# Optimization experiments

Measured on AMD Instinct MI355X. Metric: run time of the kernel, lower is better.

The kernel has to match this reference:

```python
import jax, jax.numpy as jnp
import numpy as np

N = 50000
E = 800000
F = 128


def gcn_smooth(edge_index, x):
    """Symmetric-normalized GCN smoothing: D^-1/2 (A + I) D^-1/2 x.

    edge_index: [2, E] int (src, dst) of a sparse graph; self-loops added here.
    x: [N, F] float node features.
    """
    src, dst = edge_index[0], edge_index[1]
    n = x.shape[0]
    # degree of A + I
    deg = jax.ops.segment_sum(jnp.ones((src.shape[0],), x.dtype), dst, num_segments=n) + 1.0
    dinv = jax.lax.rsqrt(deg)  # [N]
    # per-edge normalization d^-1/2[src] * d^-1/2[dst]
    norm_e = dinv[src] * dinv[dst]  # [E]
    msg = x[src] * norm_e[:, None]  # [E, F] -- gather + scale
    agg = jax.ops.segment_sum(msg, dst, num_segments=n)  # scatter-add over dst
    # self-loop contribution: dinv[i]^2 * x[i]
    return agg + (dinv * dinv)[:, None] * x


def setup_inputs() -> dict:
    key = jax.random.key(0)
    ks = jax.random.split(key, 12)
    inp = {
        "X_HypGNet": jax.random.normal(ks[0], (N, F), jnp.float32),
        "X_CGNet": jax.random.normal(ks[1], (N, F), jnp.float32),
        "X_SGNet": jax.random.normal(ks[2], (N, F), jnp.float32),
        "edge_index_hyp": jax.random.randint(ks[3], (2, E), 0, N, dtype=jnp.int32),
        "edge_index_c": jax.random.randint(ks[4], (2, E), 0, N, dtype=jnp.int32),
        "edge_index_s": jax.random.randint(ks[5], (2, E), 0, N, dtype=jnp.int32),
        "W_hyp": jax.random.normal(ks[6], (F, F), jnp.float32) * 0.05,
        "b_hyp": jax.random.normal(ks[7], (F,), jnp.float32) * 0.05,
        "W_cg": jax.random.normal(ks[8], (F, F), jnp.float32) * 0.05,
        "b_cg": jax.random.normal(ks[9], (F,), jnp.float32) * 0.05,
        "W_sg": jax.random.normal(ks[10], (F, F), jnp.float32) * 0.05,
        "b_sg": jax.random.normal(ks[11], (F,), jnp.float32) * 0.05,
    }
    return inp


def reference(X_HypGNet, X_CGNet, X_SGNet, edge_index_hyp, edge_index_c, edge_index_s,
              W_hyp, b_hyp, W_cg, b_cg, W_sg, b_sg):
    X_hyp = X_HypGNet @ W_hyp + b_hyp
    X_cg = X_CGNet @ W_cg + b_cg
    X_sg = X_SGNet @ W_sg + b_sg
    X_hyp_s = gcn_smooth(edge_index_hyp, X_hyp)
    X_cg_s = gcn_smooth(edge_index_c, X_cg)
    X_sg_s = gcn_smooth(edge_index_s, X_sg)
    return (X_hyp_s, X_cg_s, X_sg_s)
```

## Files before the change

kernel.cpp:

```cpp
#include <hip/hip_runtime.h>

#define F_DIM 128
#define NG 3
#define AEPT 16
#define CAP 48
#define MAXBIN 256
#define SPILL_CAP 8192

typedef __attribute__((ext_vector_type(8))) short short8_t;
typedef __attribute__((ext_vector_type(4))) float f32x4;

__device__ __forceinline__ unsigned short f2bf(float f) {
    unsigned int x = __float_as_uint(f);
    unsigned int r = x + 0x7fffu + ((x >> 16) & 1u);
    return (unsigned short)(r >> 16);
}
__device__ __forceinline__ float bflo(unsigned int u) { return __uint_as_float(u << 16); }
__device__ __forceinline__ float bfhi(unsigned int u) { return __uint_as_float(u & 0xffff0000u); }

__device__ __forceinline__ short8_t cvt8(float4 x0, float4 x1) {
    union { short8_t s; uint4 u; } pk;
    pk.u.x = (unsigned)f2bf(x0.x) | ((unsigned)f2bf(x0.y) << 16);
    pk.u.y = (unsigned)f2bf(x0.z) | ((unsigned)f2bf(x0.w) << 16);
    pk.u.z = (unsigned)f2bf(x1.x) | ((unsigned)f2bf(x1.y) << 16);
    pk.u.w = (unsigned)f2bf(x1.z) | ((unsigned)f2bf(x1.w) << 16);
    return pk.s;
}

struct GArgs {
    const int* src[NG]; const int* dst[NG];
    const float* X[NG]; const float* W[NG]; const float* b[NG];
    float* out[NG];
    unsigned short* Xps[NG];
    unsigned short* sorted[NG];
    unsigned short* Wtb[NG];
    int* binbuf[NG];
    int* bincur[NG];
    int* cstore[NG];
    float* dinv[NG];
    int* spill[NG];
    int* spill_n[NG];
    int nbin, bincap;
};

__global__ __launch_bounds__(256) void init_kernel(GArgs a, int g0) {
    int g = g0 + blockIdx.y;
    for (int i = threadIdx.x; i < a.nbin; i += 256) a.bincur[g][i] = i * a.bincap;
    if (threadIdx.x == 0) a.spill_n[g][0] = 0;
}

__global__ __launch_bounds__(256) void prew_kernel(GArgs a, int g0) {
    int g = g0 + blockIdx.y;
    const float* W = a.W[g];
    unsigned short* Wtb = a.Wtb[g];
    for (int i = threadIdx.x; i < 16 * 128; i += 256) {
        int kg = i >> 7, c = i & 127;
        const float* wp = W + (size_t)(kg * 8) * F_DIM + c;
        uint4 pk;
        pk.x = (unsigned)f2bf(wp[0])   | ((unsigned)f2bf(wp[128]) << 16);
        pk.y = (unsigned)f2bf(wp[256]) | ((unsigned)f2bf(wp[384]) << 16);
        pk.z = (unsigned)f2bf(wp[512]) | ((unsigned)f2bf(wp[640]) << 16);
        pk.w = (unsigned)f2bf(wp[768]) | ((unsigned)f2bf(wp[896]) << 16);
        *(uint4*)(Wtb + (size_t)i * 8) = pk;
    }
}

__global__ __launch_bounds__(256) void binA_kernel(GArgs a, int g0, int E) {
    int g = g0 + blockIdx.y;
    __shared__ int cnt[MAXBIN];
    __shared__ int lcur[MAXBIN];
    const int t = threadIdx.x;
    const int nbin = a.nbin, bincap = a.bincap;
    for (int i = t; i < nbin; i += 256) cnt[i] = 0;
    __syncthreads();
    const int* dst = a.dst[g];
    const int* src = a.src[g];
    const int base = blockIdx.x * (256 * AEPT) + t;
    int dd[AEPT], sv[AEPT];
#pragma unroll
    for (int i = 0; i < AEPT; ++i) {
        int e = base + i * 256;
        int ec = (e < E) ? e : 0;
        dd[i] = __builtin_nontemporal_load(&dst[ec]);
        sv[i] = __builtin_nontemporal_load(&src[ec]);
        if (e < E) atomicAdd(&cnt[dd[i] >> 8], 1);
    }
    __syncthreads();
    for (int i = t; i < nbin; i += 256) {
        int c = cnt[i];
        lcur[i] = c ? atomicAdd(&a.bincur[g][i], c) : 0;
    }
    __syncthreads();
    int* binbuf = a.binbuf[g];
#pragma unroll
    for (int i = 0; i < AEPT; ++i) {
        int e = base + i * 256;
        if (e < E) {
            int bin = dd[i] >> 8;
            int pos = atomicAdd(&lcur[bin], 1);
            if (pos < (bin + 1) * bincap) {
                binbuf[pos] = ((dd[i] & 255) << 16) | sv[i];
            } else {
                int sp = atomicAdd(a.spill_n[g], 1);
                if (sp < SPILL_CAP) {
                    a.spill[g][2 * sp] = sv[i];
                    a.spill[g][2 * sp + 1] = dd[i];
                }
            }
        }
    }
}

__global__ __launch_bounds__(256) void binB_kernel(GArgs a, int g0, int n) {
    int g = g0 + blockIdx.y;
    int bin = blockIdx.x;
    const int t = threadIdx.x;
    __shared__ int cnt[256];
    cnt[t] = 0;
    __syncthreads();
    const int bincap = a.bincap;
    int used = a.bincur[g][bin] - bin * bincap;
    int rd = min(used, bincap);
    const int* bb = a.binbuf[g] + bin * bincap;
    unsigned short* sorted = a.sorted[g];
    for (int j = t; j < rd; j += 256) {
        int u = bb[j];
        int dl = u >> 16;
        int s = u & 0xffff;
        int tk = atomicAdd(&cnt[dl], 1);
        int d = (bin << 8) + dl;
        if (tk < CAP) {
            sorted[d * CAP + tk] = (unsigned short)s;
        } else {
            int sp = atomicAdd(a.spill_n[g], 1);
            if (sp < SPILL_CAP) {
                a.spill[g][2 * sp] = s;
                a.spill[g][2 * sp + 1] = d;
            }
        }
    }
    __syncthreads();
    int d = (bin << 8) + t;
    if (d < n) {
        int deg = cnt[t];
        a.cstore[g][d] = min(deg, CAP);
        a.dinv[g][d] = rsqrtf((float)deg + 1.0f);
    }
}

__global__ __launch_bounds__(256) void gemm_kernel(GArgs a, int g0, int n) {
    int g = g0 + blockIdx.y;
    const int t = threadIdx.x;
    const int l = t & 63;
    const int wv = t >> 6;
    const int wr = wv >> 1, wc = wv & 1;
    const int lm = l & 15, lk = l >> 4;
    const int rowA = blockIdx.x * 128 + wr * 64 + lm;
    const float* X = a.X[g];
    const unsigned short* Wtb = a.Wtb[g];

    f32x4 acc[4][4] = {};
#pragma unroll
    for (int ks = 0; ks < 4; ++ks) {
        short8_t bv[4];
#pragma unroll
        for (int nt = 0; nt < 4; ++nt) {
            int col = wc * 64 + nt * 16 + lm;
            bv[nt] = *(const short8_t*)(Wtb + ((size_t)((ks * 4 + lk) * 128 + col)) * 8);
        }
        float4 xr[4][2];
#pragma unroll
        for (int mt = 0; mt < 4; ++mt) {
            int row = rowA + mt * 16;
            row = row < n ? row : n - 1;
            const float4* xp = (const float4*)(X + (size_t)row * F_DIM + ks * 32 + lk * 8);
            xr[mt][0] = xp[0];
            xr[mt][1] = xp[1];
        }
#pragma unroll
        for (int mt = 0; mt < 4; ++mt) {
            short8_t af = cvt8(xr[mt][0], xr[mt][1]);
#pragma unroll
            for (int nt = 0; nt < 4; ++nt)
                acc[mt][nt] = __builtin_amdgcn_mfma_f32_16x16x32_bf16(af, bv[nt],
                                                                      acc[mt][nt], 0, 0, 0);
        }
    }

    const float* bia = a.b[g];
    const float* dinv = a.dinv[g];
    unsigned short* Xps = a.Xps[g];
    const int rb = blockIdx.x * 128 + wr * 64;
#pragma unroll
    for (int nt = 0; nt < 4; ++nt) {
        int col = wc * 64 + nt * 16 + lm;
        float bc = bia[col];
#pragma unroll
        for (int mt = 0; mt < 4; ++mt) {
            int rbase = rb + mt * 16 + lk * 4;
#pragma unroll
            for (int r = 0; r < 4; ++r) {
                int row = rbase + r;
                if (row < n) {
                    float v = (acc[mt][nt][r] + bc) * dinv[row];
                    Xps[(size_t)row * F_DIM + col] = f2bf(v);
                }
            }
        }
    }
}

__global__ __launch_bounds__(256) void agg_kernel(GArgs a, int g0, int n) {
    int g = g0 + blockIdx.y;
    int wave = (blockIdx.x * 256 + threadIdx.x) >> 6;
    if (wave >= n) return;
    const int l = threadIdx.x & 63;
    const int c = l & 15;
    const int hi = l >> 4;
    const uint4* Xp4 = (const uint4*)a.Xps[g];
    const unsigned short* sorted = a.sorted[g];
    int cnt = a.cstore[g][wave];
    int s = (l < cnt) ? (int)__builtin_nontemporal_load(&sorted[(size_t)wave * CAP + l]) : 0;
    float a0 = 0.f, a1 = 0.f, a2 = 0.f, a3 = 0.f, a4 = 0.f, a5 = 0.f, a6 = 0.f, a7 = 0.f;
    for (int k = 0; k < cnt; k += 8) {
        int e0 = k + hi, e1 = k + 4 + hi;
        int s0 = __shfl(s, e0, 64);
        int s1 = __shfl(s, e1 < CAP ? e1 : 0, 64);
        uint4 v0 = Xp4[(size_t)s0 * 16 + c];
        uint4 v1 = Xp4[(size_t)s1 * 16 + c];
        if (e0 >= cnt) v0 = make_uint4(0u, 0u, 0u, 0u);
        if (e1 >= cnt) v1 = make_uint4(0u, 0u, 0u, 0u);
        a0 += bflo(v0.x); a1 += bfhi(v0.x);
        a2 += bflo(v0.y); a3 += bfhi(v0.y);
        a4 += bflo(v0.z); a5 += bfhi(v0.z);
        a6 += bflo(v0.w); a7 += bfhi(v0.w);
        a0 += bflo(v1.x); a1 += bfhi(v1.x);
        a2 += bflo(v1.y); a3 += bfhi(v1.y);
        a4 += bflo(v1.z); a5 += bfhi(v1.z);
        a6 += bflo(v1.w); a7 += bfhi(v1.w);
    }
    a0 += __shfl_xor(a0, 16, 64); a0 += __shfl_xor(a0, 32, 64);
    a1 += __shfl_xor(a1, 16, 64); a1 += __shfl_xor(a1, 32, 64);
    a2 += __shfl_xor(a2, 16, 64); a2 += __shfl_xor(a2, 32, 64);
    a3 += __shfl_xor(a3, 16, 64); a3 += __shfl_xor(a3, 32, 64);
    a4 += __shfl_xor(a4, 16, 64); a4 += __shfl_xor(a4, 32, 64);
    a5 += __shfl_xor(a5, 16, 64); a5 += __shfl_xor(a5, 32, 64);
    a6 += __shfl_xor(a6, 16, 64); a6 += __shfl_xor(a6, 32, 64);
    a7 += __shfl_xor(a7, 16, 64); a7 += __shfl_xor(a7, 32, 64);
    uint4 v = Xp4[(size_t)wave * 16 + c];
    a0 += bflo(v.x); a1 += bfhi(v.x);
    a2 += bflo(v.y); a3 += bfhi(v.y);
    a4 += bflo(v.z); a5 += bfhi(v.z);
    a6 += bflo(v.w); a7 += bfhi(v.w);
    float dd = a.dinv[g][wave];
    if (hi == 0) {
        float* o = (float*)a.out[g] + (size_t)wave * F_DIM + c * 8;
        *(float4*)(o + 0) = make_float4(a0 * dd, a1 * dd, a2 * dd, a3 * dd);
        *(float4*)(o + 4) = make_float4(a4 * dd, a5 * dd, a6 * dd, a7 * dd);
    }
}

__global__ __launch_bounds__(128) void spill_kernel(GArgs a, int g0) {
    int g = g0 + blockIdx.y;
    int ns = min(a.spill_n[g][0], SPILL_CAP);
    const unsigned short* Xps = a.Xps[g];
    const float* dinv = a.dinv[g];
    float* out = a.out[g];
    for (int i = blockIdx.x; i < ns; i += gridDim.x) {
        int s = a.spill[g][2 * i];
        int d = a.spill[g][2 * i + 1];
        float w = dinv[d];
        int f = threadIdx.x;
        float v = __uint_as_float(((unsigned int)Xps[(size_t)s * F_DIM + f]) << 16);
        unsafeAtomicAdd(&out[(size_t)d * F_DIM + f], w * v);
    }
}

extern "C" void kernel_launch(void* const* d_in, const int* in_sizes, int n_in,
                              void* d_out, int out_size, void* d_ws, size_t ws_size,
                              hipStream_t stream) {
    const float* Xin[NG] = {(const float*)d_in[0], (const float*)d_in[1], (const float*)d_in[2]};
    const int* ei[NG] = {(const int*)d_in[3], (const int*)d_in[4], (const int*)d_in[5]};
    const float* Wk[NG] = {(const float*)d_in[6], (const float*)d_in[8], (const float*)d_in[10]};
    const float* bk[NG] = {(const float*)d_in[7], (const float*)d_in[9], (const float*)d_in[11]};

    const int N = in_sizes[0] / F_DIM;
    const int E = in_sizes[3] / 2;
    float* out = (float*)d_out;

    const int nbin = (N + 255) >> 8;
    const int bincap = E / nbin + E / (3 * nbin) + 256;

    const size_t xps_b = (size_t)N * F_DIM * 2;
    const size_t sorted_b = (size_t)N * CAP * 2;
    const size_t wtb_b = (size_t)16 * 128 * 8 * 2;
    const size_t binbuf_b = (size_t)nbin * bincap * 4;
    const size_t nb = (size_t)N * 4;
    const size_t bincur_b = ((size_t)nbin * 4 + 255) / 256 * 256;
    const size_t spill_b = (size_t)SPILL_CAP * 8 + 64;
    const size_t per = ((xps_b + sorted_b + wtb_b + binbuf_b + 2 * nb + bincur_b + spill_b
                         + 255) / 256) * 256;
    const bool fused = ws_size >= (size_t)NG * per;
    char* base = (char*)d_ws;

    GArgs a;
    a.nbin = nbin;
    a.bincap = bincap;
    for (int r = 0; r < NG; ++r) {
        char* s = base + (size_t)(fused ? r : 0) * per;
        size_t off = 0;
        a.Xps[r] = (unsigned short*)(s + off); off += xps_b;
        a.sorted[r] = (unsigned short*)(s + off); off += sorted_b;
        a.Wtb[r] = (unsigned short*)(s + off); off += wtb_b;
        a.binbuf[r] = (int*)(s + off); off += binbuf_b;
        a.cstore[r] = (int*)(s + off); off += nb;
        a.dinv[r] = (float*)(s + off); off += nb;
        a.bincur[r] = (int*)(s + off); off += bincur_b;
        a.spill[r] = (int*)(s + off);
        a.spill_n[r] = (int*)(s + off + spill_b - 64);
        a.src[r] = ei[r];
        a.dst[r] = ei[r] + E;
        a.X[r] = Xin[r];
        a.W[r] = Wk[r];
        a.b[r] = bk[r];
        a.out[r] = out + (size_t)r * N * F_DIM;
    }

    const dim3 blk(256);
    const int gAe = (E + 256 * AEPT - 1) / (256 * AEPT);
    const int gR = (N + 127) / 128;
    const int gG = (N * 64 + 255) / 256;

    if (fused) {
        init_kernel<<<dim3(1, NG), blk, 0, stream>>>(a, 0);
        prew_kernel<<<dim3(1, NG), blk, 0, stream>>>(a, 0);
        binA_kernel<<<dim3(gAe, NG), blk, 0, stream>>>(a, 0, E);
        binB_kernel<<<dim3(nbin, NG), blk, 0, stream>>>(a, 0, N);
        gemm_kernel<<<dim3(gR, NG), blk, 0, stream>>>(a, 0, N);
        agg_kernel<<<dim3(gG, NG), blk, 0, stream>>>(a, 0, N);
        spill_kernel<<<dim3(16, NG), dim3(128), 0, stream>>>(a, 0);
    } else {
        for (int g = 0; g < NG; ++g) {
            init_kernel<<<dim3(1, 1), blk, 0, stream>>>(a, g);
            prew_kernel<<<dim3(1, 1), blk, 0, stream>>>(a, g);
            binA_kernel<<<dim3(gAe, 1), blk, 0, stream>>>(a, g, E);
            binB_kernel<<<dim3(nbin, 1), blk, 0, stream>>>(a, g, N);
            gemm_kernel<<<dim3(gR, 1), blk, 0, stream>>>(a, g, N);
            agg_kernel<<<dim3(gG, 1), blk, 0, stream>>>(a, g, N);
            spill_kernel<<<dim3(16, 1), dim3(128), 0, stream>>>(a, g);
        }
    }
}
```

Measured before the change: 193.0 us.

## Merge W prep into init, co-schedule binning with GEMM, move dinv[src] scaling to aggregation

W conversion is folded into the init kernel, and the edge binning and the feature GEMM now run as two block ranges of a single launch. This works because the GEMM no longer needs dinv, which is only known after binning. The source-side dinv scaling moves into the aggregation kernel, which gathers dinv[src] per edge and weights each gathered row, and the spill kernel now applies the src factor too. The aggregation loop is also unrolled to four gathers per iteration. This removes two launches and one serialization point, at the cost of extra per-edge dinv loads and multiplies in the gather loop.

Result: faster. 176.8 us (-8.4%).

```diff
diff --git a/kernel.cpp b/kernel.cpp
--- a/kernel.cpp
+++ b/kernel.cpp
@@ -47,10 +47,6 @@
     int g = g0 + blockIdx.y;
     for (int i = threadIdx.x; i < a.nbin; i += 256) a.bincur[g][i] = i * a.bincap;
     if (threadIdx.x == 0) a.spill_n[g][0] = 0;
-}
-
-__global__ __launch_bounds__(256) void prew_kernel(GArgs a, int g0) {
-    int g = g0 + blockIdx.y;
     const float* W = a.W[g];
     unsigned short* Wtb = a.Wtb[g];
     for (int i = threadIdx.x; i < 16 * 128; i += 256) {
@@ -65,46 +61,104 @@
     }
 }
 
-__global__ __launch_bounds__(256) void binA_kernel(GArgs a, int g0, int E) {
-    int g = g0 + blockIdx.y;
-    __shared__ int cnt[MAXBIN];
-    __shared__ int lcur[MAXBIN];
+__global__ __launch_bounds__(256) void work_kernel(GArgs a, int g0, int E, int n, int gA) {
+    int g = g0 + blockIdx.y;
     const int t = threadIdx.x;
-    const int nbin = a.nbin, bincap = a.bincap;
-    for (int i = t; i < nbin; i += 256) cnt[i] = 0;
-    __syncthreads();
-    const int* dst = a.dst[g];
-    const int* src = a.src[g];
-    const int base = blockIdx.x * (256 * AEPT) + t;
-    int dd[AEPT], sv[AEPT];
-#pragma unroll
-    for (int i = 0; i < AEPT; ++i) {
-        int e = base + i * 256;
-        int ec = (e < E) ? e : 0;
-        dd[i] = __builtin_nontemporal_load(&dst[ec]);
-        sv[i] = __builtin_nontemporal_load(&src[ec]);
-        if (e < E) atomicAdd(&cnt[dd[i] >> 8], 1);
-    }
-    __syncthreads();
-    for (int i = t; i < nbin; i += 256) {
-        int c = cnt[i];
-        lcur[i] = c ? atomicAdd(&a.bincur[g][i], c) : 0;
-    }
-    __syncthreads();
-    int* binbuf = a.binbuf[g];
-#pragma unroll
-    for (int i = 0; i < AEPT; ++i) {
-        int e = base + i * 256;
-        if (e < E) {
-            int bin = dd[i] >> 8;
-            int pos = atomicAdd(&lcur[bin], 1);
-            if (pos < (bin + 1) * bincap) {
-                binbuf[pos] = ((dd[i] & 255) << 16) | sv[i];
-            } else {
-                int sp = atomicAdd(a.spill_n[g], 1);
-                if (sp < SPILL_CAP) {
-                    a.spill[g][2 * sp] = sv[i];
-                    a.spill[g][2 * sp + 1] = dd[i];
+    if ((int)blockIdx.x < gA) {
+        __shared__ int cnt[MAXBIN];
+        __shared__ int lcur[MAXBIN];
+        const int nbin = a.nbin, bincap = a.bincap;
+        for (int i = t; i < nbin; i += 256) cnt[i] = 0;
+        __syncthreads();
+        const int* dst = a.dst[g];
+        const int* src = a.src[g];
+        const int base = blockIdx.x * (256 * AEPT) + t;
+        int dd[AEPT], sv[AEPT];
+#pragma unroll
+        for (int i = 0; i < AEPT; ++i) {
+            int e = base + i * 256;
+            int ec = (e < E) ? e : 0;
+            dd[i] = __builtin_nontemporal_load(&dst[ec]);
+            sv[i] = __builtin_nontemporal_load(&src[ec]);
+            if (e < E) atomicAdd(&cnt[dd[i] >> 8], 1);
+        }
+        __syncthreads();
+        for (int i = t; i < nbin; i += 256) {
+            int c = cnt[i];
+            lcur[i] = c ? atomicAdd(&a.bincur[g][i], c) : 0;
+        }
+        __syncthreads();
+        int* binbuf = a.binbuf[g];
+#pragma unroll
+        for (int i = 0; i < AEPT; ++i) {
+            int e = base + i * 256;
+            if (e < E) {
+                int bin = dd[i] >> 8;
+                int pos = atomicAdd(&lcur[bin], 1);
+                if (pos < (bin + 1) * bincap) {
+                    binbuf[pos] = ((dd[i] & 255) << 16) | sv[i];
+                } else {
+                    int sp = atomicAdd(a.spill_n[g], 1);
+                    if (sp < SPILL_CAP) {
+                        a.spill[g][2 * sp] = sv[i];
+                        a.spill[g][2 * sp + 1] = dd[i];
+                    }
+                }
+            }
+        }
+    } else {
+        const int bx = blockIdx.x - gA;
+        const int l = t & 63;
+        const int wv = t >> 6;
+        const int wr = wv >> 1, wc = wv & 1;
+        const int lm = l & 15, lk = l >> 4;
+        const int rowA = bx * 128 + wr * 64 + lm;
+        const float* X = a.X[g];
+        const unsigned short* Wtb = a.Wtb[g];
+
+        f32x4 acc[4][4] = {};
+#pragma unroll
+        for (int ks = 0; ks < 4; ++ks) {
+            short8_t bv[4];
+#pragma unroll
+            for (int nt = 0; nt < 4; ++nt) {
+                int col = wc * 64 + nt * 16 + lm;
+                bv[nt] = *(const short8_t*)(Wtb + ((size_t)((ks * 4 + lk) * 128 + col)) * 8);
+            }
+            float4 xr[4][2];
+#pragma unroll
+            for (int mt = 0; mt < 4; ++mt) {
+                int row = rowA + mt * 16;
+                row = row < n ? row : n - 1;
+                const float4* xp = (const float4*)(X + (size_t)row * F_DIM + ks * 32 + lk * 8);
+                xr[mt][0] = xp[0];
+                xr[mt][1] = xp[1];
+            }
+#pragma unroll
+            for (int mt = 0; mt < 4; ++mt) {
+                short8_t af = cvt8(xr[mt][0], xr[mt][1]);
+#pragma unroll
+                for (int nt = 0; nt < 4; ++nt)
+                    acc[mt][nt] = __builtin_amdgcn_mfma_f32_16x16x32_bf16(af, bv[nt],
+                                                                          acc[mt][nt], 0, 0, 0);
+            }
+        }
+
+        const float* bia = a.b[g];
+        unsigned short* Xps = a.Xps[g];
+        const int rb = bx * 128 + wr * 64;
+#pragma unroll
+        for (int nt = 0; nt < 4; ++nt) {
+            int col = wc * 64 + nt * 16 + lm;
+            float bc = bia[col];
+#pragma unroll
+            for (int mt = 0; mt < 4; ++mt) {
+                int rbase = rb + mt * 16 + lk * 4;
+#pragma unroll
+                for (int r = 0; r < 4; ++r) {
+                    int row = rbase + r;
+                    if (row < n)
+                        Xps[(size_t)row * F_DIM + col] = f2bf(acc[mt][nt][r] + bc);
                 }
             }
         }
@@ -148,68 +202,6 @@
     }
 }
 
-__global__ __launch_bounds__(256) void gemm_kernel(GArgs a, int g0, int n) {
-    int g = g0 + blockIdx.y;
-    const int t = threadIdx.x;
-    const int l = t & 63;
-    const int wv = t >> 6;
-    const int wr = wv >> 1, wc = wv & 1;
-    const int lm = l & 15, lk = l >> 4;
-    const int rowA = blockIdx.x * 128 + wr * 64 + lm;
-    const float* X = a.X[g];
-    const unsigned short* Wtb = a.Wtb[g];
-
-    f32x4 acc[4][4] = {};
-#pragma unroll
-    for (int ks = 0; ks < 4; ++ks) {
-        short8_t bv[4];
-#pragma unroll
-        for (int nt = 0; nt < 4; ++nt) {
-            int col = wc * 64 + nt * 16 + lm;
-            bv[nt] = *(const short8_t*)(Wtb + ((size_t)((ks * 4 + lk) * 128 + col)) * 8);
-        }
-        float4 xr[4][2];
-#pragma unroll
-        for (int mt = 0; mt < 4; ++mt) {
-            int row = rowA + mt * 16;
-            row = row < n ? row : n - 1;
-            const float4* xp = (const float4*)(X + (size_t)row * F_DIM + ks * 32 + lk * 8);
-            xr[mt][0] = xp[0];
-            xr[mt][1] = xp[1];
-        }
-#pragma unroll
-        for (int mt = 0; mt < 4; ++mt) {
-            short8_t af = cvt8(xr[mt][0], xr[mt][1]);
-#pragma unroll
-            for (int nt = 0; nt < 4; ++nt)
-                acc[mt][nt] = __builtin_amdgcn_mfma_f32_16x16x32_bf16(af, bv[nt],
-                                                                      acc[mt][nt], 0, 0, 0);
-        }
-    }
-
-    const float* bia = a.b[g];
-    const float* dinv = a.dinv[g];
-    unsigned short* Xps = a.Xps[g];
-    const int rb = blockIdx.x * 128 + wr * 64;
-#pragma unroll
-    for (int nt = 0; nt < 4; ++nt) {
-        int col = wc * 64 + nt * 16 + lm;
-        float bc = bia[col];
-#pragma unroll
-        for (int mt = 0; mt < 4; ++mt) {
-            int rbase = rb + mt * 16 + lk * 4;
-#pragma unroll
-            for (int r = 0; r < 4; ++r) {
-                int row = rbase + r;
-                if (row < n) {
-                    float v = (acc[mt][nt][r] + bc) * dinv[row];
-                    Xps[(size_t)row * F_DIM + col] = f2bf(v);
-                }
-            }
-        }
-    }
-}
-
 __global__ __launch_bounds__(256) void agg_kernel(GArgs a, int g0, int n) {
     int g = g0 + blockIdx.y;
     int wave = (blockIdx.x * 256 + threadIdx.x) >> 6;
@@ -219,25 +211,49 @@
     const int hi = l >> 4;
     const uint4* Xp4 = (const uint4*)a.Xps[g];
     const unsigned short* sorted = a.sorted[g];
+    const float* dinv = a.dinv[g];
     int cnt = a.cstore[g][wave];
-    int s = (l < cnt) ? (int)__builtin_nontemporal_load(&sorted[(size_t)wave * CAP + l]) : 0;
+    int s = 0;
+    float dv = 0.f;
+    if (l < cnt) {
+        s = (int)__builtin_nontemporal_load(&sorted[(size_t)wave * CAP + l]);
+        dv = dinv[s];
+    }
     float a0 = 0.f, a1 = 0.f, a2 = 0.f, a3 = 0.f, a4 = 0.f, a5 = 0.f, a6 = 0.f, a7 = 0.f;
-    for (int k = 0; k < cnt; k += 8) {
-        int e0 = k + hi, e1 = k + 4 + hi;
+    for (int k = 0; k < cnt; k += 16) {
+        int e0 = k + hi, e1 = k + 4 + hi, e2 = k + 8 + hi, e3 = k + 12 + hi;
         int s0 = __shfl(s, e0, 64);
-        int s1 = __shfl(s, e1 < CAP ? e1 : 0, 64);
+        int s1 = __shfl(s, e1, 64);
+        int s2 = __shfl(s, e2, 64);
+        int s3 = __shfl(s, e3, 64);
+        float w0 = __shfl(dv, e0, 64);
+        float w1 = __shfl(dv, e1, 64);
+        float w2 = __shfl(dv, e2, 64);
+        float w3 = __shfl(dv, e3, 64);
         uint4 v0 = Xp4[(size_t)s0 * 16 + c];
         uint4 v1 = Xp4[(size_t)s1 * 16 + c];
-        if (e0 >= cnt) v0 = make_uint4(0u, 0u, 0u, 0u);
-        if (e1 >= cnt) v1 = make_uint4(0u, 0u, 0u, 0u);
-        a0 += bflo(v0.x); a1 += bfhi(v0.x);
-        a2 += bflo(v0.y); a3 += bfhi(v0.y);
-        a4 += bflo(v0.z); a5 += bfhi(v0.z);
-        a6 += bflo(v0.w); a7 += bfhi(v0.w);
-        a0 += bflo(v1.x); a1 += bfhi(v1.x);
-        a2 += bflo(v1.y); a3 += bfhi(v1.y);
-        a4 += bflo(v1.z); a5 += bfhi(v1.z);
-        a6 += bflo(v1.w); a7 += bfhi(v1.w);
+        uint4 v2 = Xp4[(size_t)s2 * 16 + c];
+        uint4 v3 = Xp4[(size_t)s3 * 16 + c];
+        if (e0 >= cnt) w0 = 0.f;
+        if (e1 >= cnt) w1 = 0.f;
+        if (e2 >= cnt) w2 = 0.f;
+        if (e3 >= cnt) w3 = 0.f;
+        a0 += bflo(v0.x) * w0; a1 += bfhi(v0.x) * w0;
+        a2 += bflo(v0.y) * w0; a3 += bfhi(v0.y) * w0;
+        a4 += bflo(v0.z) * w0; a5 += bfhi(v0.z) * w0;
+        a6 += bflo(v0.w) * w0; a7 += bfhi(v0.w) * w0;
+        a0 += bflo(v1.x) * w1; a1 += bfhi(v1.x) * w1;
+        a2 += bflo(v1.y) * w1; a3 += bfhi(v1.y) * w1;
+        a4 += bflo(v1.z) * w1; a5 += bfhi(v1.z) * w1;
+        a6 += bflo(v1.w) * w1; a7 += bfhi(v1.w) * w1;
+        a0 += bflo(v2.x) * w2; a1 += bfhi(v2.x) * w2;
+        a2 += bflo(v2.y) * w2; a3 += bfhi(v2.y) * w2;
+        a4 += bflo(v2.z) * w2; a5 += bfhi(v2.z) * w2;
+        a6 += bflo(v2.w) * w2; a7 += bfhi(v2.w) * w2;
+        a0 += bflo(v3.x) * w3; a1 += bfhi(v3.x) * w3;
+        a2 += bflo(v3.y) * w3; a3 += bfhi(v3.y) * w3;
+        a4 += bflo(v3.z) * w3; a5 += bfhi(v3.z) * w3;
+        a6 += bflo(v3.w) * w3; a7 += bfhi(v3.w) * w3;
     }
     a0 += __shfl_xor(a0, 16, 64); a0 += __shfl_xor(a0, 32, 64);
     a1 += __shfl_xor(a1, 16, 64); a1 += __shfl_xor(a1, 32, 64);
@@ -247,12 +263,12 @@
     a5 += __shfl_xor(a5, 16, 64); a5 += __shfl_xor(a5, 32, 64);
     a6 += __shfl_xor(a6, 16, 64); a6 += __shfl_xor(a6, 32, 64);
     a7 += __shfl_xor(a7, 16, 64); a7 += __shfl_xor(a7, 32, 64);
+    float dd = dinv[wave];
     uint4 v = Xp4[(size_t)wave * 16 + c];
-    a0 += bflo(v.x); a1 += bfhi(v.x);
-    a2 += bflo(v.y); a3 += bfhi(v.y);
-    a4 += bflo(v.z); a5 += bfhi(v.z);
-    a6 += bflo(v.w); a7 += bfhi(v.w);
-    float dd = a.dinv[g][wave];
+    a0 += bflo(v.x) * dd; a1 += bfhi(v.x) * dd;
+    a2 += bflo(v.y) * dd; a3 += bfhi(v.y) * dd;
+    a4 += bflo(v.z) * dd; a5 += bfhi(v.z) * dd;
+    a6 += bflo(v.w) * dd; a7 += bfhi(v.w) * dd;
     if (hi == 0) {
         float* o = (float*)a.out[g] + (size_t)wave * F_DIM + c * 8;
         *(float4*)(o + 0) = make_float4(a0 * dd, a1 * dd, a2 * dd, a3 * dd);
@@ -269,7 +285,7 @@
     for (int i = blockIdx.x; i < ns; i += gridDim.x) {
         int s = a.spill[g][2 * i];
         int d = a.spill[g][2 * i + 1];
-        float w = dinv[d];
+        float w = dinv[d] * dinv[s];
         int f = threadIdx.x;
         float v = __uint_as_float(((unsigned int)Xps[(size_t)s * F_DIM + f]) << 16);
         unsafeAtomicAdd(&out[(size_t)d * F_DIM + f], w * v);
@@ -333,19 +349,15 @@
 
     if (fused) {
         init_kernel<<<dim3(1, NG), blk, 0, stream>>>(a, 0);
-        prew_kernel<<<dim3(1, NG), blk, 0, stream>>>(a, 0);
-        binA_kernel<<<dim3(gAe, NG), blk, 0, stream>>>(a, 0, E);
+        work_kernel<<<dim3(gAe + gR, NG), blk, 0, stream>>>(a, 0, E, N, gAe);
         binB_kernel<<<dim3(nbin, NG), blk, 0, stream>>>(a, 0, N);
-        gemm_kernel<<<dim3(gR, NG), blk, 0, stream>>>(a, 0, N);
         agg_kernel<<<dim3(gG, NG), blk, 0, stream>>>(a, 0, N);
         spill_kernel<<<dim3(16, NG), dim3(128), 0, stream>>>(a, 0);
     } else {
         for (int g = 0; g < NG; ++g) {
             init_kernel<<<dim3(1, 1), blk, 0, stream>>>(a, g);
-            prew_kernel<<<dim3(1, 1), blk, 0, stream>>>(a, g);
-            binA_kernel<<<dim3(gAe, 1), blk, 0, stream>>>(a, g, E);
+            work_kernel<<<dim3(gAe + gR, 1), blk, 0, stream>>>(a, g, E, N, gAe);
             binB_kernel<<<dim3(nbin, 1), blk, 0, stream>>>(a, g, N);
-            gemm_kernel<<<dim3(gR, 1), blk, 0, stream>>>(a, g, N);
             agg_kernel<<<dim3(gG, 1), blk, 0, stream>>>(a, g, N);
             spill_kernel<<<dim3(16, 1), dim3(128), 0, stream>>>(a, g);
         }
```
